# Performance work log

Hardware: AMD Instinct MI355X
Metric: run time of the kernel (lower is better)

The kernel has to match this reference:

```python
import math
import jax, jax.numpy as jnp
import numpy as np

NH, D, MULT, VOCAB, NLAYER = 4, 256, 128, 256, 2
N = MULT * D // NH  # 8192
EPS = 1e-5
THETA = 2.0 ** 16


def get_freqs(n):
    q = (jnp.arange(n, dtype=jnp.float32) // 2) * 2  # quantize(t, 2)
    return 1.0 / (THETA ** (q / n)) / (2 * math.pi)


def ln(x):
    # LayerNorm over last dim, no affine
    mu = jnp.mean(x, axis=-1, keepdims=True)
    var = jnp.mean((x - mu) ** 2, axis=-1, keepdims=True)
    return (x - mu) / jnp.sqrt(var + EPS)


def rope(phases, v):
    # phases: (T, N), v: (B, nh, T, N)
    ph = (phases % 1.0) * (2 * math.pi)
    c, s = jnp.cos(ph), jnp.sin(ph)
    v_rot = jnp.stack((-v[..., 1::2], v[..., ::2]), axis=-1).reshape(v.shape)
    return v * c + v_rot * s


def setup_inputs() -> dict:
    key = jax.random.key(0)
    ks = jax.random.split(key, 6)
    std = 0.02
    return {
        "idx": jax.random.randint(ks[0], (1, 2048), 0, VOCAB),
        "embed": jax.random.normal(ks[1], (VOCAB, D), jnp.float32) * std,
        "encoder": jax.random.normal(ks[2], (NH, D, N), jnp.float32) * std,
        "encoder_v": jax.random.normal(ks[3], (NH, D, N), jnp.float32) * std,
        "decoder": jax.random.normal(ks[4], (NH * N, D), jnp.float32) * std,
        "lm_head": jax.random.normal(ks[5], (D, VOCAB), jnp.float32) * std,
    }


def reference(idx, embed, encoder, encoder_v, decoder, lm_head):
    B, T = idx.shape
    freqs = get_freqs(N)  # (N,)
    phases = jnp.arange(T, dtype=jnp.float32)[:, None] * freqs[None, :]  # (T, N)
    # strictly-lower-triangular causal mask (tril diagonal=-1)
    t = jnp.arange(T)
    mask = (t[:, None] > t[None, :]).astype(jnp.float32)  # (T, T)

    x = ln(embed[idx][:, None])  # (B, 1, T, D)
    for _ in range(NLAYER):
        x_sparse = jax.nn.relu(jnp.einsum('bltd,hdn->bhtn', x, encoder))  # (B,nh,T,N)
        QR = rope(phases, x_sparse)
        scores = jnp.einsum('bhtn,bhsn->bhts', QR, QR) * mask  # (B,nh,T,T)
        yKV = ln(jnp.einsum('bhts,blsd->bhtd', scores, x))  # (B,nh,T,D)
        y_sparse = jax.nn.relu(jnp.einsum('bhtd,hdn->bhtn', yKV, encoder_v))
        xy = x_sparse * y_sparse  # (B,nh,T,N)
        xy = xy.transpose(0, 2, 1, 3).reshape(B, 1, T, NH * N)
        yMLP = xy @ decoder  # (B,1,T,D)
        x = ln(x + ln(yMLP))
    logits = x[:, 0] @ lm_head  # (B,T,vocab)
    return logits
```

## Files before the change

kernel.cpp:

```cpp
#include <hip/hip_runtime.h>
#include <hip/hip_bf16.h>
#include <math.h>

typedef unsigned short u16;
typedef unsigned int u32;
typedef __attribute__((ext_vector_type(8))) short short8;
typedef __attribute__((ext_vector_type(4))) float f32x4;

__device__ __forceinline__ u16 f2b(float f) {
  u32 u = __builtin_bit_cast(u32, f);
  u = (u + 0x7fffu + ((u >> 16) & 1u)) >> 16;
  return (u16)u;
}
__device__ __forceinline__ float b2f(u16 s) {
  return __builtin_bit_cast(float, (u32)s << 16);
}

__device__ __forceinline__ void ld_g2l(const u16* g, u16* l) {
  __builtin_amdgcn_global_load_lds(
      (const __attribute__((address_space(1))) unsigned int*)g,
      (__attribute__((address_space(3))) unsigned int*)l, 16, 0, 0);
}

__device__ __forceinline__ float rope_frev(int n) {
  return exp2f((float)(-(n & ~1)) * (1.0f / 512.0f)) * 0.15915494f;
}
__device__ __forceinline__ void rope_cs_fast(float frev, int t, float& c, float& s) {
  float ph = (float)t * frev;
  ph -= floorf(ph);
#if __has_builtin(__builtin_amdgcn_sinf) && __has_builtin(__builtin_amdgcn_cosf)
  s = __builtin_amdgcn_sinf(ph);
  c = __builtin_amdgcn_cosf(ph);
#else
  __sincosf(ph * 6.2831853f, &s, &c);
#endif
}

__device__ __forceinline__ void gemm_core(
    const u16* __restrict__ A, const u16* __restrict__ B,
    int lda, int ldb, int Klen, int kb, int bm, int bn,
    u16* __restrict__ As, u16* __restrict__ Bs, f32x4 (&acc)[4][4])
{
  int tid = threadIdx.x;
  int w = tid >> 6, lane = tid & 63;
  int srow = (w << 4) + (lane >> 2);
  int scol = (lane & 3) << 3;
  const u16* ga0 = A + (long)(bm * 128 + srow) * lda + kb + scol;
  const u16* ga1 = ga0 + (long)64 * lda;
  const u16* gb0 = B + (long)(bn * 128 + srow) * ldb + kb + scol;
  const u16* gb1 = gb0 + (long)64 * ldb;
  u16* la0 = As + (w << 9);  u16* la1 = la0 + 2048;
  u16* lb0 = Bs + (w << 9);  u16* lb1 = lb0 + 2048;

  int wm = (w >> 1) << 6, wn = (w & 1) << 6;
  int lane15 = lane & 15, quad = lane >> 4;
  const u16* ar = As + (wm + lane15) * 32 + quad * 8;
  const u16* br = Bs + (wn + lane15) * 32 + quad * 8;

#pragma unroll
  for (int i = 0; i < 4; i++)
#pragma unroll
    for (int j = 0; j < 4; j++) { f32x4 z = {0.f, 0.f, 0.f, 0.f}; acc[i][j] = z; }

  for (int k = 0; k < Klen; k += 64) {
    ld_g2l(ga0 + k, la0);
    ld_g2l(ga1 + k, la1);
    ld_g2l(gb0 + k, lb0);
    ld_g2l(gb1 + k, lb1);
    ld_g2l(ga0 + k + 32, la0 + 4096);
    ld_g2l(ga1 + k + 32, la1 + 4096);
    ld_g2l(gb0 + k + 32, lb0 + 4096);
    ld_g2l(gb1 + k + 32, lb1 + 4096);
    __syncthreads();
#pragma unroll
    for (int h = 0; h < 2; h++) {
      short8 af[4], bfr[4];
#pragma unroll
      for (int mt = 0; mt < 4; mt++) af[mt] = *(const short8*)(ar + h * 4096 + mt * 16 * 32);
#pragma unroll
      for (int nt = 0; nt < 4; nt++) bfr[nt] = *(const short8*)(br + h * 4096 + nt * 16 * 32);
#pragma unroll
      for (int mt = 0; mt < 4; mt++)
#pragma unroll
        for (int nt = 0; nt < 4; nt++)
          acc[mt][nt] = __builtin_amdgcn_mfma_f32_16x16x32_bf16(af[mt], bfr[nt], acc[mt][nt], 0, 0, 0);
    }
    __syncthreads();
  }
}

template<int EPI>
__global__ __launch_bounds__(256, 2) void gemm_bt(
    const u16* __restrict__ A, const u16* __restrict__ B, void* __restrict__ C,
    int K, int lda, int ldb, int ldc, int nsplits, long aB, long bB, long cB,
    int tri)
{
  __shared__ __align__(16) u16 As[2 * 128 * 32];
  __shared__ __align__(16) u16 Bs[2 * 128 * 32];
  int bn = blockIdx.x, bm = blockIdx.y;
  int batch = blockIdx.z / nsplits, sp = blockIdx.z % nsplits;
  int Klen = K / nsplits, kb = sp * Klen;
  if (tri) {
    int kend = (bm + 1) * 128;
    if (kb >= kend) return;
    if (kb + Klen > kend) Klen = kend - kb;
  }

  f32x4 acc[4][4];
  gemm_core(A + (long)batch * aB, B + (long)batch * bB, lda, ldb, Klen, kb, bm, bn, As, Bs, acc);

  int lane = threadIdx.x & 63, w = threadIdx.x >> 6;
  int wm = (w >> 1) << 6, wn = (w & 1) << 6;
  int lane15 = lane & 15, quad = lane >> 4;

  float frev[4] = {0.f, 0.f, 0.f, 0.f};
  if (EPI == 1 || EPI == 4) {
#pragma unroll
    for (int nt = 0; nt < 4; nt++)
      frev[nt] = rope_frev(bn * 128 + wn + nt * 16 + lane15);
  }

#pragma unroll
  for (int mt = 0; mt < 4; mt++)
#pragma unroll
    for (int nt = 0; nt < 4; nt++) {
      int gn = bn * 128 + wn + nt * 16 + lane15;
#pragma unroll
      for (int r = 0; r < 4; r++) {
        int gm = bm * 128 + wm + mt * 16 + quad * 4 + r;
        float v = acc[mt][nt][r];
        long ci = (long)batch * cB + (long)gm * ldc + gn;
        if (EPI == 0) {
          ((float*)C)[ci] = v;
        } else if (EPI == 1) {
          float rv = fmaxf(v, 0.f);
          float ro = __shfl_xor(rv, 1);
          float c, s; rope_cs_fast(frev[nt], gm, c, s);
          float out = (gn & 1) ? (rv * c + ro * s) : (rv * c - ro * s);
          ((u16*)C)[ci] = f2b(out);
        } else if (EPI == 3) {
          atomicAdd(&((float*)C)[ci], v);
        } else if (EPI == 4) {
          u16* Cp = (u16*)C;
          float q = b2f(Cp[ci]);
          float qo = __shfl_xor(q, 1);
          float c, s; rope_cs_fast(frev[nt], gm, c, s);
          float xs = (gn & 1) ? (q * c - qo * s) : (q * c + qo * s);
          Cp[ci] = f2b(fmaxf(v, 0.f) * xs);
        }
      }
    }
}

#define SC_BAR   __builtin_amdgcn_s_barrier()
#define SC_LGKM0 asm volatile("s_waitcnt lgkmcnt(0)" ::: "memory")
#define SC_LGKM8 asm volatile("s_waitcnt lgkmcnt(8)" ::: "memory")
#define SC_VMF   do { asm volatile("s_waitcnt vmcnt(4)" ::: "memory"); \
                      __builtin_amdgcn_sched_barrier(0); } while (0)
#define SC_P1    __builtin_amdgcn_s_setprio(1)
#define SC_P0    __builtin_amdgcn_s_setprio(0)

#define DSA(Ab, mh) { \
  _Pragma("unroll") for (int mt = 0; mt < 4; mt++) { \
    aA[mt][0] = *(const short8*)((Ab) + ((mh) * 64 + mt * 16) * 64 + koff0); \
    aA[mt][1] = *(const short8*)((Ab) + ((mh) * 64 + mt * 16) * 64 + koff1); } }

#define DSB(Bb, nh, dst) { \
  _Pragma("unroll") for (int nt = 0; nt < 2; nt++) { \
    dst[nt][0] = *(const short8*)((Bb) + ((nh) * 32 + nt * 16) * 64 + koff0); \
    dst[nt][1] = *(const short8*)((Bb) + ((nh) * 32 + nt * 16) * 64 + koff1); } }

#define MMA(MH, NH, BB) { \
  _Pragma("unroll") for (int mt = 0; mt < 4; mt++) \
  _Pragma("unroll") for (int nt = 0; nt < 2; nt++) { \
    acc[(MH)*4+mt][(NH)*2+nt] = __builtin_amdgcn_mfma_f32_16x16x32_bf16( \
        aA[mt][0], BB[nt][0], acc[(MH)*4+mt][(NH)*2+nt], 0, 0, 0); \
    acc[(MH)*4+mt][(NH)*2+nt] = __builtin_amdgcn_mfma_f32_16x16x32_bf16( \
        aA[mt][1], BB[nt][1], acc[(MH)*4+mt][(NH)*2+nt], 0, 0, 0); } }

__global__ __launch_bounds__(512, 1) void gemm_scores8(
    const u16* __restrict__ QR, u16* __restrict__ S, int T, int ntri)
{
  __shared__ __align__(16) u16 Abuf[2][256 * 64];
  __shared__ __align__(16) u16 Bbuf[2][256 * 64];

  int total = gridDim.x;
  int lin = blockIdx.x;
  int cpx = total >> 3, rr = total & 7;
  int xcd = lin & 7, ii = lin >> 3;
  int c = (xcd < rr) ? xcd * (cpx + 1) + ii
                     : rr * (cpx + 1) + (xcd - rr) * cpx + ii;
  int zh = c / ntri, q = c % ntri;

  int bm = (int)((sqrtf(8.f * (float)q + 1.f) - 1.f) * 0.5f);
  while ((bm + 1) * (bm + 2) / 2 <= q) bm++;
  while (bm * (bm + 1) / 2 > q) bm--;
  int bn = q - bm * (bm + 1) / 2;

  const u16* Q = QR + (long)zh * (long)T * 8192;
  u16* Sb = S + (long)zh * (long)T * T;

  int tid = threadIdx.x;
  int w = tid >> 6, lane = tid & 63;
  int wr = w >> 2, wc = w & 3;
  int lane15 = lane & 15, quad = lane >> 4;
  int swz = lane15 & 7;
  int koff0 = ((quad) ^ swz) << 3;
  int koff1 = ((4 + quad) ^ swz) << 3;

  const u16* gA = Q + (long)(bm * 256) * 8192;
  const u16* gB = Q + (long)(bn * 256) * 8192;

  const u16* A0 = &Abuf[0][(wr * 128 + lane15) * 64];
  const u16* A1 = &Abuf[1][(wr * 128 + lane15) * 64];
  const u16* B0 = &Bbuf[0][(wc * 64 + lane15) * 64];
  const u16* B1 = &Bbuf[1][(wc * 64 + lane15) * 64];

  int sr = lane >> 3, sc = lane & 7;
  long g_sk = (long)sr * 8192 + ((sc ^ sr) << 3);
  int l_base = (w * 16) * 64;
  long g_wrow = (long)(w * 16) * 8192;

  auto STG = [&](const u16* gHalfBase, u16* lHalfBase, int kt) {
    const u16* g = gHalfBase + g_wrow + g_sk + kt * 64;
    u16* l = lHalfBase + l_base;
    ld_g2l(g, l);
    ld_g2l(g + (long)8 * 8192, l + 8 * 64);
  };

  f32x4 acc[8][4];
#pragma unroll
  for (int i2 = 0; i2 < 8; i2++)
#pragma unroll
    for (int j = 0; j < 4; j++) { f32x4 z = {0.f, 0.f, 0.f, 0.f}; acc[i2][j] = z; }

  const long HSTEP = (long)128 * 8192;

  STG(gA, &Abuf[0][0], 0); STG(gA + HSTEP, &Abuf[0][128 * 64], 0);
  STG(gB, &Bbuf[0][0], 0); STG(gB + HSTEP, &Bbuf[0][128 * 64], 0);
  STG(gB, &Bbuf[1][0], 1); STG(gB + HSTEP, &Bbuf[1][128 * 64], 1);
  SC_VMF;
  SC_BAR;

  const int nkt = 8192 / 64;
  for (int i = 0; i < nkt / 2; i++) {
    int kt1 = 2 * i + 1;
    int kt2 = 2 * i + 2; if (kt2 > nkt - 1) kt2 = nkt - 1;
    int kt3 = 2 * i + 3; if (kt3 > nkt - 1) kt3 = nkt - 1;
    short8 aA[4][2], bb0[2][2], bb1[2][2];

    DSA(A0, 0); DSB(B0, 0, bb0);
    STG(gA, &Abuf[1][0], kt1);
    SC_LGKM8; SC_BAR; SC_LGKM0; SC_P1; MMA(0, 0, bb0); SC_P0; SC_BAR;
    DSB(B0, 1, bb1);
    STG(gA + HSTEP, &Abuf[1][128 * 64], kt1);
    SC_BAR; SC_LGKM0; SC_P1; MMA(0, 1, bb1); SC_P0; SC_BAR;
    DSA(A0, 1);
    STG(gB, &Bbuf[0][0], kt2);
    SC_BAR; SC_LGKM0; SC_P1; MMA(1, 1, bb1); SC_P0; SC_BAR;
    STG(gB + HSTEP, &Bbuf[0][128 * 64], kt2);
    SC_VMF; SC_BAR; SC_LGKM0; SC_P1; MMA(1, 0, bb0); SC_P0; SC_BAR;

    DSA(A1, 0); DSB(B1, 0, bb0);
    STG(gA, &Abuf[0][0], kt2);
    SC_LGKM8; SC_BAR; SC_LGKM0; SC_P1; MMA(0, 0, bb0); SC_P0; SC_BAR;
    DSB(B1, 1, bb1);
    STG(gA + HSTEP, &Abuf[0][128 * 64], kt2);
    SC_BAR; SC_LGKM0; SC_P1; MMA(0, 1, bb1); SC_P0; SC_BAR;
    DSA(A1, 1);
    STG(gB, &Bbuf[1][0], kt3);
    SC_BAR; SC_LGKM0; SC_P1; MMA(1, 1, bb1); SC_P0; SC_BAR;
    STG(gB + HSTEP, &Bbuf[1][128 * 64], kt3);
    SC_VMF; SC_BAR; SC_LGKM0; SC_P1; MMA(1, 0, bb0); SC_P0; SC_BAR;
  }

#pragma unroll
  for (int mt = 0; mt < 8; mt++)
#pragma unroll
    for (int nt = 0; nt < 4; nt++) {
      int gn = bn * 256 + wc * 64 + nt * 16 + lane15;
#pragma unroll
      for (int r = 0; r < 4; r++) {
        int gm = bm * 256 + wr * 128 + mt * 16 + quad * 4 + r;
        Sb[(long)gm * T + gn] = f2b(gm > gn ? acc[mt][nt][r] : 0.f);
      }
    }
}

__global__ __launch_bounds__(256) void trans_f32_bf16(
    const float* __restrict__ src, u16* __restrict__ dst, int R, int C)
{
  __shared__ float tile[32][33];
  long off = (long)blockIdx.z * R * C;
  const float* s = src + off;
  u16* d = dst + off;
  int lx = threadIdx.x & 31, ly = threadIdx.x >> 5;
  int c = blockIdx.x * 32 + lx;
#pragma unroll
  for (int p = 0; p < 32; p += 8)
    tile[ly + p][lx] = s[(long)(blockIdx.y * 32 + ly + p) * C + c];
  __syncthreads();
  int rr = blockIdx.y * 32 + lx;
#pragma unroll
  for (int p = 0; p < 32; p += 8)
    d[(long)(blockIdx.x * 32 + ly + p) * R + rr] = f2b(tile[lx][ly + p]);
}

__device__ __forceinline__ float block_sum(float v, float* red) {
#pragma unroll
  for (int o = 32; o > 0; o >>= 1) v += __shfl_down(v, o, 64);
  int lane = threadIdx.x & 63, wid = threadIdx.x >> 6;
  if (lane == 0) red[wid] = v;
  __syncthreads();
  float r = red[0] + red[1] + red[2] + red[3];
  __syncthreads();
  return r;
}

__global__ __launch_bounds__(256) void embed_ln(
    const int* __restrict__ idx, const float* __restrict__ embed,
    float* __restrict__ x, u16* __restrict__ xb, u16* __restrict__ xT, int T)
{
  __shared__ float red[4];
  int t = blockIdx.x, d = threadIdx.x;
  float v = embed[(long)idx[t] * 256 + d];
  float mu = block_sum(v, red) * (1.f / 256.f);
  float c = v - mu;
  float var = block_sum(c * c, red) * (1.f / 256.f);
  float o = c * rsqrtf(var + 1e-5f);
  x[(long)t * 256 + d] = o;
  xb[(long)t * 256 + d] = f2b(o);
  xT[(long)d * T + t] = f2b(o);
}

__global__ __launch_bounds__(256) void row_ln(
    const float* __restrict__ in, u16* __restrict__ out)
{
  __shared__ float red[4];
  long row = blockIdx.x;
  int d = threadIdx.x;
  float v = in[row * 256 + d];
  float mu = block_sum(v, red) * (1.f / 256.f);
  float c = v - mu;
  float var = block_sum(c * c, red) * (1.f / 256.f);
  out[row * 256 + d] = f2b(c * rsqrtf(var + 1e-5f));
}

__global__ __launch_bounds__(256) void resid_ln(
    const float* __restrict__ yMLP, float* __restrict__ x,
    u16* __restrict__ xb, u16* __restrict__ xT, int T)
{
  __shared__ float red[4];
  int t = blockIdx.x, d = threadIdx.x;
  float y = yMLP[(long)t * 256 + d];
  float mu1 = block_sum(y, red) * (1.f / 256.f);
  float c1 = y - mu1;
  float var1 = block_sum(c1 * c1, red) * (1.f / 256.f);
  float l1 = c1 * rsqrtf(var1 + 1e-5f);
  float v = x[(long)t * 256 + d] + l1;
  float mu2 = block_sum(v, red) * (1.f / 256.f);
  float c2 = v - mu2;
  float var2 = block_sum(c2 * c2, red) * (1.f / 256.f);
  float o = c2 * rsqrtf(var2 + 1e-5f);
  x[(long)t * 256 + d] = o;
  xb[(long)t * 256 + d] = f2b(o);
  xT[(long)d * T + t] = f2b(o);
}

extern "C" void kernel_launch(void* const* d_in, const int* in_sizes, int n_in,
                              void* d_out, int out_size, void* d_ws, size_t ws_size,
                              hipStream_t stream) {
  const int*   idx       = (const int*)d_in[0];
  const float* embed     = (const float*)d_in[1];
  const float* encoder   = (const float*)d_in[2];
  const float* encoder_v = (const float*)d_in[3];
  const float* decoder   = (const float*)d_in[4];
  const float* lm_head   = (const float*)d_in[5];
  const int T = in_sizes[0];
  const int D = 256, NH = 4, Nn = 8192, V = 256;

  char* ws = (char*)d_ws;
  size_t off = 0;
  auto alloc = [&](size_t bytes) -> void* {
    void* p = ws + off; off += (bytes + 255) & ~(size_t)255; return p;
  };
  float* x_f32   = (float*)alloc((size_t)T * D * 4);
  float* yMLP    = (float*)alloc((size_t)T * D * 4);
  float* yKV_f32 = (float*)alloc((size_t)NH * T * D * 4);
  u16* x_b    = (u16*)alloc((size_t)T * D * 2);
  u16* xT     = (u16*)alloc((size_t)T * D * 2);
  u16* yKV_b  = (u16*)alloc((size_t)NH * T * D * 2);
  u16* lmT    = (u16*)alloc((size_t)D * V * 2);
  u16* encT   = (u16*)alloc((size_t)NH * Nn * D * 2);
  u16* encvT  = (u16*)alloc((size_t)NH * Nn * D * 2);
  u16* decT   = (u16*)alloc((size_t)D * NH * Nn * 2);
  size_t per_head = ((size_t)T * T * 2 + 256) + ((size_t)T * Nn * 2 + 256);
  int HB = 4;
  while (HB > 1 && off + (size_t)HB * per_head > ws_size) HB >>= 1;
  u16* scores = (u16*)alloc((size_t)HB * T * T * 2);
  u16* QRxy   = (u16*)alloc((size_t)HB * T * Nn * 2);
  if (off > ws_size) return;

  trans_f32_bf16<<<dim3(Nn / 32, D / 32, NH), 256, 0, stream>>>(encoder, encT, D, Nn);
  trans_f32_bf16<<<dim3(Nn / 32, D / 32, NH), 256, 0, stream>>>(encoder_v, encvT, D, Nn);
  trans_f32_bf16<<<dim3(D / 32, (NH * Nn) / 32, 1), 256, 0, stream>>>(decoder, decT, NH * Nn, D);
  trans_f32_bf16<<<dim3(V / 32, D / 32, 1), 256, 0, stream>>>(lm_head, lmT, D, V);

  embed_ln<<<T, 256, 0, stream>>>(idx, embed, x_f32, x_b, xT, T);

  const int nbm = T / 256, ntri = nbm * (nbm + 1) / 2;

  for (int l = 0; l < 2; l++) {
    hipMemsetAsync(yMLP, 0, (size_t)T * D * 4, stream);
    for (int h0 = 0; h0 < NH; h0 += HB) {
      gemm_bt<1><<<dim3(Nn / 128, T / 128, HB), 256, 0, stream>>>(
          x_b, encT + (size_t)h0 * Nn * D, QRxy,
          D, D, D, Nn, 1, 0L, (long)Nn * D, (long)T * Nn, 0);
      gemm_scores8<<<dim3(ntri * HB, 1, 1), 512, 0, stream>>>(QRxy, scores, T, ntri);
      hipMemsetAsync(yKV_f32, 0, (size_t)HB * T * D * 4, stream);
      gemm_bt<3><<<dim3(D / 128, T / 128, HB * 8), 256, 0, stream>>>(
          scores, xT, yKV_f32,
          T, T, T, D, 8, (long)T * T, 0L, (long)T * D, 1);
      row_ln<<<HB * T, 256, 0, stream>>>(yKV_f32, yKV_b);
      gemm_bt<4><<<dim3(Nn / 128, T / 128, HB), 256, 0, stream>>>(
          yKV_b, encvT + (size_t)h0 * Nn * D, QRxy,
          D, D, D, Nn, 1, (long)T * D, (long)Nn * D, (long)T * Nn, 0);
      gemm_bt<3><<<dim3(D / 128, T / 128, HB * 4), 256, 0, stream>>>(
          QRxy, decT + (size_t)h0 * Nn, yMLP,
          Nn, Nn, NH * Nn, D, 4, (long)T * Nn, (long)Nn, 0L, 0);
    }
    resid_ln<<<T, 256, 0, stream>>>(yMLP, x_f32, x_b, xT, T);
  }

  gemm_bt<0><<<dim3(V / 128, T / 128, 1), 256, 0, stream>>>(
      x_b, lmT, d_out, D, D, D, V, 1, 0L, 0L, 0L, 0);
}
```

Before: 1.138 ms.

## Split causal score GEMM into 128x256 tiles plus half-size diagonal tiles

The scores kernel now tiles each head's lower triangle as 64 off-diagonal 128x256 tiles plus 8 diagonal 128x128 tiles, instead of 36 256x256 tiles. This doubles the number of blocks, which should fill more of the compute units and balance load better. It also skips some work above the diagonal. In exchange, each block has a smaller A tile and less register-level reuse, and the templated core adds a second code path with different wait counts.

Result: slower. 1.233 ms (+8.3%).

```diff
diff --git a/kernel.cpp b/kernel.cpp
--- a/kernel.cpp
+++ b/kernel.cpp
@@ -155,136 +155,148 @@
 #define SC_BAR   __builtin_amdgcn_s_barrier()
 #define SC_LGKM0 asm volatile("s_waitcnt lgkmcnt(0)" ::: "memory")
 #define SC_LGKM8 asm volatile("s_waitcnt lgkmcnt(8)" ::: "memory")
-#define SC_VMF   do { asm volatile("s_waitcnt vmcnt(4)" ::: "memory"); \
-                      __builtin_amdgcn_sched_barrier(0); } while (0)
 #define SC_P1    __builtin_amdgcn_s_setprio(1)
 #define SC_P0    __builtin_amdgcn_s_setprio(0)
 
-#define DSA(Ab, mh) { \
-  _Pragma("unroll") for (int mt = 0; mt < 4; mt++) { \
-    aA[mt][0] = *(const short8*)((Ab) + ((mh) * 64 + mt * 16) * 64 + koff0); \
-    aA[mt][1] = *(const short8*)((Ab) + ((mh) * 64 + mt * 16) * 64 + koff1); } }
-
-#define DSB(Bb, nh, dst) { \
-  _Pragma("unroll") for (int nt = 0; nt < 2; nt++) { \
-    dst[nt][0] = *(const short8*)((Bb) + ((nh) * 32 + nt * 16) * 64 + koff0); \
-    dst[nt][1] = *(const short8*)((Bb) + ((nh) * 32 + nt * 16) * 64 + koff1); } }
-
-#define MMA(MH, NH, BB) { \
-  _Pragma("unroll") for (int mt = 0; mt < 4; mt++) \
-  _Pragma("unroll") for (int nt = 0; nt < 2; nt++) { \
-    acc[(MH)*4+mt][(NH)*2+nt] = __builtin_amdgcn_mfma_f32_16x16x32_bf16( \
-        aA[mt][0], BB[nt][0], acc[(MH)*4+mt][(NH)*2+nt], 0, 0, 0); \
-    acc[(MH)*4+mt][(NH)*2+nt] = __builtin_amdgcn_mfma_f32_16x16x32_bf16( \
-        aA[mt][1], BB[nt][1], acc[(MH)*4+mt][(NH)*2+nt], 0, 0, 0); } }
-
-__global__ __launch_bounds__(512, 1) void gemm_scores8(
-    const u16* __restrict__ QR, u16* __restrict__ S, int T, int ntri)
-{
-  __shared__ __align__(16) u16 Abuf[2][256 * 64];
+template<int NW>
+__device__ __forceinline__ void score_core(
+    const u16* __restrict__ gA, const u16* __restrict__ gB,
+    u16* __restrict__ Sb, int T, int rowBase, int colBase,
+    u16* __restrict__ Ab, u16* __restrict__ Bb)
+{
+  constexpr int MT = (NW == 256) ? 4 : 2;
+  constexpr int RW = (NW == 256) ? 64 : 32;
+  constexpr int WCN = NW / 64;
+
+  int tid = threadIdx.x, w = tid >> 6, lane = tid & 63;
+  int wc = w % WCN, wr = w / WCN;
+  int lane15 = lane & 15, quad = lane >> 4;
+  int swz = lane15 & 7;
+  int koff0 = (quad ^ swz) << 3;
+  int koff1 = ((4 + quad) ^ swz) << 3;
+
+  u16* A0 = Ab;               u16* A1 = Ab + 128 * 64;
+  u16* B0 = Bb;               u16* B1 = Bb + 256 * 64;
+  const u16* a0r = A0 + (wr * RW + lane15) * 64;
+  const u16* a1r = A1 + (wr * RW + lane15) * 64;
+  const u16* b0r = B0 + (wc * 64 + lane15) * 64;
+  const u16* b1r = B1 + (wc * 64 + lane15) * 64;
+
+  int sr = lane >> 3, sc = lane & 7;
+  long g_sk = (long)sr * 8192 + ((sc ^ sr) << 3);
+  int l_base = (w * 16) * 64;
+  long g_wrow = (long)(w * 16) * 8192;
+
+  auto STG = [&](const u16* gBase, u16* lBase, int kt) {
+    const u16* g = gBase + g_wrow + g_sk + (long)kt * 64;
+    u16* l = lBase + l_base;
+    ld_g2l(g, l);
+    ld_g2l(g + (long)8 * 8192, l + 8 * 64);
+  };
+
+#define SC_VMF do { if (NW == 256) { \
+    asm volatile("s_waitcnt vmcnt(4)" ::: "memory"); } else { \
+    asm volatile("s_waitcnt vmcnt(2)" ::: "memory"); } \
+    __builtin_amdgcn_sched_barrier(0); } while (0)
+
+#define RD_A(ar_) { _Pragma("unroll") for (int mt = 0; mt < MT; mt++) { \
+    aA[mt][0] = *(const short8*)((ar_) + mt * 16 * 64 + koff0); \
+    aA[mt][1] = *(const short8*)((ar_) + mt * 16 * 64 + koff1); } }
+
+#define RD_B(br_, nh_, dst) { _Pragma("unroll") for (int nt = 0; nt < 2; nt++) { \
+    dst[nt][0] = *(const short8*)((br_) + ((nh_) * 32 + nt * 16) * 64 + koff0); \
+    dst[nt][1] = *(const short8*)((br_) + ((nh_) * 32 + nt * 16) * 64 + koff1); } }
+
+#define MMA9(NH_, KF_, BB_) { _Pragma("unroll") for (int mt = 0; mt < MT; mt++) \
+    _Pragma("unroll") for (int nt = 0; nt < 2; nt++) \
+      acc[mt][(NH_) * 2 + nt] = __builtin_amdgcn_mfma_f32_16x16x32_bf16( \
+          aA[mt][KF_], BB_[nt][KF_], acc[mt][(NH_) * 2 + nt], 0, 0, 0); }
+
+  f32x4 acc[MT][4];
+#pragma unroll
+  for (int i = 0; i < MT; i++)
+#pragma unroll
+    for (int j = 0; j < 4; j++) { f32x4 z = {0.f, 0.f, 0.f, 0.f}; acc[i][j] = z; }
+
+  const long HS = (long)128 * 8192;
+
+  STG(gA, A0, 0);
+  STG(gB, B0, 0); if (NW == 256) STG(gB + HS, B0 + 128 * 64, 0);
+  STG(gB, B1, 1); if (NW == 256) STG(gB + HS, B1 + 128 * 64, 1);
+  SC_VMF;
+  SC_BAR;
+
+  for (int i = 0; i < 64; i++) {
+    int kt1 = 2 * i + 1;
+    int kt2 = 2 * i + 2; if (kt2 > 127) kt2 = 127;
+    int kt3 = 2 * i + 3; if (kt3 > 127) kt3 = 127;
+    short8 aA[MT][2], bb0[2][2], bb1[2][2];
+
+    RD_A(a0r); RD_B(b0r, 0, bb0);
+    STG(gA, A1, kt1);
+    SC_LGKM8; SC_BAR; SC_LGKM0; SC_P1; MMA9(0, 0, bb0); SC_P0; SC_BAR;
+    RD_B(b0r, 1, bb1);
+    SC_BAR; SC_LGKM0; SC_P1; MMA9(1, 0, bb1); SC_P0; SC_BAR;
+    STG(gB, B0, kt2);
+    SC_BAR; SC_P1; MMA9(1, 1, bb1); SC_P0; SC_BAR;
+    if (NW == 256) STG(gB + HS, B0 + 128 * 64, kt2);
+    SC_VMF; SC_BAR; SC_P1; MMA9(0, 1, bb0); SC_P0; SC_BAR;
+
+    RD_A(a1r); RD_B(b1r, 0, bb0);
+    STG(gA, A0, kt2);
+    SC_LGKM8; SC_BAR; SC_LGKM0; SC_P1; MMA9(0, 0, bb0); SC_P0; SC_BAR;
+    RD_B(b1r, 1, bb1);
+    SC_BAR; SC_LGKM0; SC_P1; MMA9(1, 0, bb1); SC_P0; SC_BAR;
+    STG(gB, B1, kt3);
+    SC_BAR; SC_P1; MMA9(1, 1, bb1); SC_P0; SC_BAR;
+    if (NW == 256) STG(gB + HS, B1 + 128 * 64, kt3);
+    SC_VMF; SC_BAR; SC_P1; MMA9(0, 1, bb0); SC_P0; SC_BAR;
+  }
+
+#pragma unroll
+  for (int mt = 0; mt < MT; mt++)
+#pragma unroll
+    for (int nt4 = 0; nt4 < 4; nt4++) {
+      int gn = colBase + wc * 64 + nt4 * 16 + lane15;
+#pragma unroll
+      for (int r = 0; r < 4; r++) {
+        int gm = rowBase + wr * RW + mt * 16 + quad * 4 + r;
+        Sb[(long)gm * T + gn] = f2b(gm > gn ? acc[mt][nt4][r] : 0.f);
+      }
+    }
+#undef SC_VMF
+#undef RD_A
+#undef RD_B
+#undef MMA9
+}
+
+__global__ __launch_bounds__(512, 1) void gemm_scores9(
+    const u16* __restrict__ QR, u16* __restrict__ S, int T)
+{
+  __shared__ __align__(16) u16 Abuf[2][128 * 64];
   __shared__ __align__(16) u16 Bbuf[2][256 * 64];
 
-  int total = gridDim.x;
-  int lin = blockIdx.x;
+  int total = gridDim.x, lin = blockIdx.x;
   int cpx = total >> 3, rr = total & 7;
   int xcd = lin & 7, ii = lin >> 3;
   int c = (xcd < rr) ? xcd * (cpx + 1) + ii
                      : rr * (cpx + 1) + (xcd - rr) * cpx + ii;
-  int zh = c / ntri, q = c % ntri;
-
-  int bm = (int)((sqrtf(8.f * (float)q + 1.f) - 1.f) * 0.5f);
-  while ((bm + 1) * (bm + 2) / 2 <= q) bm++;
-  while (bm * (bm + 1) / 2 > q) bm--;
-  int bn = q - bm * (bm + 1) / 2;
-
-  const u16* Q = QR + (long)zh * (long)T * 8192;
-  u16* Sb = S + (long)zh * (long)T * T;
-
-  int tid = threadIdx.x;
-  int w = tid >> 6, lane = tid & 63;
-  int wr = w >> 2, wc = w & 3;
-  int lane15 = lane & 15, quad = lane >> 4;
-  int swz = lane15 & 7;
-  int koff0 = ((quad) ^ swz) << 3;
-  int koff1 = ((4 + quad) ^ swz) << 3;
-
-  const u16* gA = Q + (long)(bm * 256) * 8192;
-  const u16* gB = Q + (long)(bn * 256) * 8192;
-
-  const u16* A0 = &Abuf[0][(wr * 128 + lane15) * 64];
-  const u16* A1 = &Abuf[1][(wr * 128 + lane15) * 64];
-  const u16* B0 = &Bbuf[0][(wc * 64 + lane15) * 64];
-  const u16* B1 = &Bbuf[1][(wc * 64 + lane15) * 64];
-
-  int sr = lane >> 3, sc = lane & 7;
-  long g_sk = (long)sr * 8192 + ((sc ^ sr) << 3);
-  int l_base = (w * 16) * 64;
-  long g_wrow = (long)(w * 16) * 8192;
-
-  auto STG = [&](const u16* gHalfBase, u16* lHalfBase, int kt) {
-    const u16* g = gHalfBase + g_wrow + g_sk + kt * 64;
-    u16* l = lHalfBase + l_base;
-    ld_g2l(g, l);
-    ld_g2l(g + (long)8 * 8192, l + 8 * 64);
-  };
-
-  f32x4 acc[8][4];
-#pragma unroll
-  for (int i2 = 0; i2 < 8; i2++)
-#pragma unroll
-    for (int j = 0; j < 4; j++) { f32x4 z = {0.f, 0.f, 0.f, 0.f}; acc[i2][j] = z; }
-
-  const long HSTEP = (long)128 * 8192;
-
-  STG(gA, &Abuf[0][0], 0); STG(gA + HSTEP, &Abuf[0][128 * 64], 0);
-  STG(gB, &Bbuf[0][0], 0); STG(gB + HSTEP, &Bbuf[0][128 * 64], 0);
-  STG(gB, &Bbuf[1][0], 1); STG(gB + HSTEP, &Bbuf[1][128 * 64], 1);
-  SC_VMF;
-  SC_BAR;
-
-  const int nkt = 8192 / 64;
-  for (int i = 0; i < nkt / 2; i++) {
-    int kt1 = 2 * i + 1;
-    int kt2 = 2 * i + 2; if (kt2 > nkt - 1) kt2 = nkt - 1;
-    int kt3 = 2 * i + 3; if (kt3 > nkt - 1) kt3 = nkt - 1;
-    short8 aA[4][2], bb0[2][2], bb1[2][2];
-
-    DSA(A0, 0); DSB(B0, 0, bb0);
-    STG(gA, &Abuf[1][0], kt1);
-    SC_LGKM8; SC_BAR; SC_LGKM0; SC_P1; MMA(0, 0, bb0); SC_P0; SC_BAR;
-    DSB(B0, 1, bb1);
-    STG(gA + HSTEP, &Abuf[1][128 * 64], kt1);
-    SC_BAR; SC_LGKM0; SC_P1; MMA(0, 1, bb1); SC_P0; SC_BAR;
-    DSA(A0, 1);
-    STG(gB, &Bbuf[0][0], kt2);
-    SC_BAR; SC_LGKM0; SC_P1; MMA(1, 1, bb1); SC_P0; SC_BAR;
-    STG(gB + HSTEP, &Bbuf[0][128 * 64], kt2);
-    SC_VMF; SC_BAR; SC_LGKM0; SC_P1; MMA(1, 0, bb0); SC_P0; SC_BAR;
-
-    DSA(A1, 0); DSB(B1, 0, bb0);
-    STG(gA, &Abuf[0][0], kt2);
-    SC_LGKM8; SC_BAR; SC_LGKM0; SC_P1; MMA(0, 0, bb0); SC_P0; SC_BAR;
-    DSB(B1, 1, bb1);
-    STG(gA + HSTEP, &Abuf[0][128 * 64], kt2);
-    SC_BAR; SC_LGKM0; SC_P1; MMA(0, 1, bb1); SC_P0; SC_BAR;
-    DSA(A1, 1);
-    STG(gB, &Bbuf[1][0], kt3);
-    SC_BAR; SC_LGKM0; SC_P1; MMA(1, 1, bb1); SC_P0; SC_BAR;
-    STG(gB + HSTEP, &Bbuf[1][128 * 64], kt3);
-    SC_VMF; SC_BAR; SC_LGKM0; SC_P1; MMA(1, 0, bb0); SC_P0; SC_BAR;
-  }
-
-#pragma unroll
-  for (int mt = 0; mt < 8; mt++)
-#pragma unroll
-    for (int nt = 0; nt < 4; nt++) {
-      int gn = bn * 256 + wc * 64 + nt * 16 + lane15;
-#pragma unroll
-      for (int r = 0; r < 4; r++) {
-        int gm = bm * 256 + wr * 128 + mt * 16 + quad * 4 + r;
-        Sb[(long)gm * T + gn] = f2b(gm > gn ? acc[mt][nt][r] : 0.f);
-      }
-    }
+  int head = c / 72, r72 = c % 72;
+
+  const u16* Q = QR + (long)head * (long)T * 8192;
+  u16* Sb = S + (long)head * (long)T * T;
+
+  if (r72 < 8) {
+    int n = r72;
+    score_core<128>(Q + (long)n * 256 * 8192, Q + (long)n * 256 * 8192,
+                    Sb, T, n * 256, n * 256, &Abuf[0][0], &Bbuf[0][0]);
+  } else {
+    int L = r72 - 8, n = 0;
+    while (L >= 15 - 2 * n) { L -= 15 - 2 * n; n++; }
+    int mrow = 2 * n + 1 + L;
+    score_core<256>(Q + (long)mrow * 128 * 8192, Q + (long)n * 256 * 8192,
+                    Sb, T, mrow * 128, n * 256, &Abuf[0][0], &Bbuf[0][0]);
+  }
 }
 
 __global__ __launch_bounds__(256) void trans_f32_bf16(
@@ -408,15 +420,13 @@
 
   embed_ln<<<T, 256, 0, stream>>>(idx, embed, x_f32, x_b, xT, T);
 
-  const int nbm = T / 256, ntri = nbm * (nbm + 1) / 2;
-
   for (int l = 0; l < 2; l++) {
     hipMemsetAsync(yMLP, 0, (size_t)T * D * 4, stream);
     for (int h0 = 0; h0 < NH; h0 += HB) {
       gemm_bt<1><<<dim3(Nn / 128, T / 128, HB), 256, 0, stream>>>(
           x_b, encT + (size_t)h0 * Nn * D, QRxy,
           D, D, D, Nn, 1, 0L, (long)Nn * D, (long)T * Nn, 0);
-      gemm_scores8<<<dim3(ntri * HB, 1, 1), 512, 0, stream>>>(QRxy, scores, T, ntri);
+      gemm_scores9<<<dim3(HB * 72, 1, 1), 512, 0, stream>>>(QRxy, scores, T);
       hipMemsetAsync(yKV_f32, 0, (size_t)HB * T * D * 4, stream);
       gemm_bt<3><<<dim3(D / 128, T / 128, HB * 8), 256, 0, stream>>>(
           scores, xT, yKV_f32,
```

## Split scores GEMM along K into three slices with fp32 atomic accumulation

Applied to the files above, without the earlier changes.

Adds a split-K variant of the causal scores GEMM. Each 256x256 lower-triangle tile is computed by three blocks covering K slices of 44/44/40 k-tiles, which accumulate into a zeroed fp32 buffer with atomicAdd. A separate kernel then applies the strict causal mask and converts to bf16. With T=2048 and HB=4 there are only 36*4=144 tile blocks at one block per CU, so the split is meant to fill the CUs better. The cost is an extra fp32 T×T buffer, a memset, atomic traffic and a conversion pass, and the result now depends on atomic ordering.

New measurement: 1.140 ms. Within noise of the previous version (+0.2%).

```diff
diff --git a/kernel.cpp b/kernel.cpp
--- a/kernel.cpp
+++ b/kernel.cpp
@@ -6,6 +6,7 @@
 typedef unsigned int u32;
 typedef __attribute__((ext_vector_type(8))) short short8;
 typedef __attribute__((ext_vector_type(4))) float f32x4;
+typedef __attribute__((ext_vector_type(4))) unsigned short u16x4;
 
 __device__ __forceinline__ u16 f2b(float f) {
   u32 u = __builtin_bit_cast(u32, f);
@@ -178,63 +179,103 @@
     acc[(MH)*4+mt][(NH)*2+nt] = __builtin_amdgcn_mfma_f32_16x16x32_bf16( \
         aA[mt][1], BB[nt][1], acc[(MH)*4+mt][(NH)*2+nt], 0, 0, 0); } }
 
+#define SCORES_K_LOOP(kb, nkt) \
+  for (int i = 0; i < (nkt) / 2; i++) { \
+    int kt1 = (kb) + 2 * i + 1; \
+    int kt2 = 2 * i + 2; if (kt2 > (nkt) - 1) kt2 = (nkt) - 1; kt2 += (kb); \
+    int kt3 = 2 * i + 3; if (kt3 > (nkt) - 1) kt3 = (nkt) - 1; kt3 += (kb); \
+    short8 aA[4][2], bb0[2][2], bb1[2][2]; \
+     \
+    DSA(A0, 0); DSB(B0, 0, bb0); \
+    STG(gA, &Abuf[1][0], kt1); \
+    SC_LGKM8; SC_BAR; SC_LGKM0; SC_P1; MMA(0, 0, bb0); SC_P0; SC_BAR; \
+     \
+    DSB(B0, 1, bb1); \
+    STG(gA + HSTEP, &Abuf[1][128 * 64], kt1); \
+    SC_BAR; SC_LGKM0; SC_P1; MMA(0, 1, bb1); SC_P0; SC_BAR; \
+     \
+    DSA(A0, 1); \
+    STG(gB, &Bbuf[0][0], kt2); \
+    SC_BAR; SC_LGKM0; SC_P1; MMA(1, 1, bb1); SC_P0; SC_BAR; \
+     \
+    STG(gB + HSTEP, &Bbuf[0][128 * 64], kt2); \
+    SC_VMF; SC_BAR; SC_LGKM0; SC_P1; MMA(1, 0, bb0); SC_P0; SC_BAR; \
+     \
+    DSA(A1, 0); DSB(B1, 0, bb0); \
+    STG(gA, &Abuf[0][0], kt2); \
+    SC_LGKM8; SC_BAR; SC_LGKM0; SC_P1; MMA(0, 0, bb0); SC_P0; SC_BAR; \
+     \
+    DSB(B1, 1, bb1); \
+    STG(gA + HSTEP, &Abuf[0][128 * 64], kt2); \
+    SC_BAR; SC_LGKM0; SC_P1; MMA(0, 1, bb1); SC_P0; SC_BAR; \
+     \
+    DSA(A1, 1); \
+    STG(gB, &Bbuf[1][0], kt3); \
+    SC_BAR; SC_LGKM0; SC_P1; MMA(1, 1, bb1); SC_P0; SC_BAR; \
+     \
+    STG(gB + HSTEP, &Bbuf[1][128 * 64], kt3); \
+    SC_VMF; SC_BAR; SC_LGKM0; SC_P1; MMA(1, 0, bb0); SC_P0; SC_BAR; \
+  }
+
+#define SCORES_SETUP \
+  int tid = threadIdx.x; \
+  int w = tid >> 6, lane = tid & 63; \
+  int wr = w >> 2, wc = w & 3; \
+  int lane15 = lane & 15, quad = lane >> 4; \
+  int swz = lane15 & 7; \
+  int koff0 = ((quad) ^ swz) << 3; \
+  int koff1 = ((4 + quad) ^ swz) << 3; \
+  const u16* gA = Q + (long)(bm * 256) * 8192; \
+  const u16* gB = Q + (long)(bn * 256) * 8192; \
+  const u16* A0 = &Abuf[0][(wr * 128 + lane15) * 64]; \
+  const u16* A1 = &Abuf[1][(wr * 128 + lane15) * 64]; \
+  const u16* B0 = &Bbuf[0][(wc * 64 + lane15) * 64]; \
+  const u16* B1 = &Bbuf[1][(wc * 64 + lane15) * 64]; \
+  int sr = lane >> 3, sc = lane & 7; \
+  long g_sk = (long)sr * 8192 + ((sc ^ sr) << 3); \
+  int l_base = (w * 16) * 64; \
+  long g_wrow = (long)(w * 16) * 8192; \
+  auto STG = [&](const u16* gHalfBase, u16* lHalfBase, int kt) { \
+    const u16* g = gHalfBase + g_wrow + g_sk + (long)kt * 64; \
+    u16* l = lHalfBase + l_base; \
+    ld_g2l(g, l); \
+    ld_g2l(g + (long)8 * 8192, l + 8 * 64); \
+  }; \
+  f32x4 acc[8][4]; \
+  _Pragma("unroll") \
+  for (int i2 = 0; i2 < 8; i2++) \
+  _Pragma("unroll") \
+    for (int j = 0; j < 4; j++) { f32x4 z = {0.f, 0.f, 0.f, 0.f}; acc[i2][j] = z; } \
+  const long HSTEP = (long)128 * 8192;
+
+__device__ __forceinline__ void tri_decode(int q, int& bm, int& bn) {
+  bm = (int)((sqrtf(8.f * (float)q + 1.f) - 1.f) * 0.5f);
+  while ((bm + 1) * (bm + 2) / 2 <= q) bm++;
+  while (bm * (bm + 1) / 2 > q) bm--;
+  bn = q - bm * (bm + 1) / 2;
+}
+
+__device__ __forceinline__ int xcd_remap(int lin, int total) {
+  int cpx = total >> 3, rr = total & 7;
+  int xcd = lin & 7, ii = lin >> 3;
+  return (xcd < rr) ? xcd * (cpx + 1) + ii
+                    : rr * (cpx + 1) + (xcd - rr) * cpx + ii;
+}
+
 __global__ __launch_bounds__(512, 1) void gemm_scores8(
     const u16* __restrict__ QR, u16* __restrict__ S, int T, int ntri)
 {
   __shared__ __align__(16) u16 Abuf[2][256 * 64];
   __shared__ __align__(16) u16 Bbuf[2][256 * 64];
 
-  int total = gridDim.x;
-  int lin = blockIdx.x;
-  int cpx = total >> 3, rr = total & 7;
-  int xcd = lin & 7, ii = lin >> 3;
-  int c = (xcd < rr) ? xcd * (cpx + 1) + ii
-                     : rr * (cpx + 1) + (xcd - rr) * cpx + ii;
+  int c = xcd_remap(blockIdx.x, gridDim.x);
   int zh = c / ntri, q = c % ntri;
-
-  int bm = (int)((sqrtf(8.f * (float)q + 1.f) - 1.f) * 0.5f);
-  while ((bm + 1) * (bm + 2) / 2 <= q) bm++;
-  while (bm * (bm + 1) / 2 > q) bm--;
-  int bn = q - bm * (bm + 1) / 2;
+  int bm, bn; tri_decode(q, bm, bn);
 
   const u16* Q = QR + (long)zh * (long)T * 8192;
   u16* Sb = S + (long)zh * (long)T * T;
 
-  int tid = threadIdx.x;
-  int w = tid >> 6, lane = tid & 63;
-  int wr = w >> 2, wc = w & 3;
-  int lane15 = lane & 15, quad = lane >> 4;
-  int swz = lane15 & 7;
-  int koff0 = ((quad) ^ swz) << 3;
-  int koff1 = ((4 + quad) ^ swz) << 3;
-
-  const u16* gA = Q + (long)(bm * 256) * 8192;
-  const u16* gB = Q + (long)(bn * 256) * 8192;
-
-  const u16* A0 = &Abuf[0][(wr * 128 + lane15) * 64];
-  const u16* A1 = &Abuf[1][(wr * 128 + lane15) * 64];
-  const u16* B0 = &Bbuf[0][(wc * 64 + lane15) * 64];
-  const u16* B1 = &Bbuf[1][(wc * 64 + lane15) * 64];
-
-  int sr = lane >> 3, sc = lane & 7;
-  long g_sk = (long)sr * 8192 + ((sc ^ sr) << 3);
-  int l_base = (w * 16) * 64;
-  long g_wrow = (long)(w * 16) * 8192;
-
-  auto STG = [&](const u16* gHalfBase, u16* lHalfBase, int kt) {
-    const u16* g = gHalfBase + g_wrow + g_sk + kt * 64;
-    u16* l = lHalfBase + l_base;
-    ld_g2l(g, l);
-    ld_g2l(g + (long)8 * 8192, l + 8 * 64);
-  };
-
-  f32x4 acc[8][4];
-#pragma unroll
-  for (int i2 = 0; i2 < 8; i2++)
-#pragma unroll
-    for (int j = 0; j < 4; j++) { f32x4 z = {0.f, 0.f, 0.f, 0.f}; acc[i2][j] = z; }
-
-  const long HSTEP = (long)128 * 8192;
+  SCORES_SETUP
 
   STG(gA, &Abuf[0][0], 0); STG(gA + HSTEP, &Abuf[0][128 * 64], 0);
   STG(gB, &Bbuf[0][0], 0); STG(gB + HSTEP, &Bbuf[0][128 * 64], 0);
@@ -242,37 +283,7 @@
   SC_VMF;
   SC_BAR;
 
-  const int nkt = 8192 / 64;
-  for (int i = 0; i < nkt / 2; i++) {
-    int kt1 = 2 * i + 1;
-    int kt2 = 2 * i + 2; if (kt2 > nkt - 1) kt2 = nkt - 1;
-    int kt3 = 2 * i + 3; if (kt3 > nkt - 1) kt3 = nkt - 1;
-    short8 aA[4][2], bb0[2][2], bb1[2][2];
-
-    DSA(A0, 0); DSB(B0, 0, bb0);
-    STG(gA, &Abuf[1][0], kt1);
-    SC_LGKM8; SC_BAR; SC_LGKM0; SC_P1; MMA(0, 0, bb0); SC_P0; SC_BAR;
-    DSB(B0, 1, bb1);
-    STG(gA + HSTEP, &Abuf[1][128 * 64], kt1);
-    SC_BAR; SC_LGKM0; SC_P1; MMA(0, 1, bb1); SC_P0; SC_BAR;
-    DSA(A0, 1);
-    STG(gB, &Bbuf[0][0], kt2);
-    SC_BAR; SC_LGKM0; SC_P1; MMA(1, 1, bb1); SC_P0; SC_BAR;
-    STG(gB + HSTEP, &Bbuf[0][128 * 64], kt2);
-    SC_VMF; SC_BAR; SC_LGKM0; SC_P1; MMA(1, 0, bb0); SC_P0; SC_BAR;
-
-    DSA(A1, 0); DSB(B1, 0, bb0);
-    STG(gA, &Abuf[0][0], kt2);
-    SC_LGKM8; SC_BAR; SC_LGKM0; SC_P1; MMA(0, 0, bb0); SC_P0; SC_BAR;
-    DSB(B1, 1, bb1);
-    STG(gA + HSTEP, &Abuf[0][128 * 64], kt2);
-    SC_BAR; SC_LGKM0; SC_P1; MMA(0, 1, bb1); SC_P0; SC_BAR;
-    DSA(A1, 1);
-    STG(gB, &Bbuf[1][0], kt3);
-    SC_BAR; SC_LGKM0; SC_P1; MMA(1, 1, bb1); SC_P0; SC_BAR;
-    STG(gB + HSTEP, &Bbuf[1][128 * 64], kt3);
-    SC_VMF; SC_BAR; SC_LGKM0; SC_P1; MMA(1, 0, bb0); SC_P0; SC_BAR;
-  }
+  SCORES_K_LOOP(0, 128)
 
 #pragma unroll
   for (int mt = 0; mt < 8; mt++)
@@ -285,6 +296,71 @@
         Sb[(long)gm * T + gn] = f2b(gm > gn ? acc[mt][nt][r] : 0.f);
       }
     }
+}
+
+__global__ __launch_bounds__(512, 1) void gemm_scores_k3(
+    const u16* __restrict__ QR, float* __restrict__ Sf, int T, int ntri)
+{
+  __shared__ __align__(16) u16 Abuf[2][256 * 64];
+  __shared__ __align__(16) u16 Bbuf[2][256 * 64];
+
+  int c = xcd_remap(blockIdx.x, gridDim.x);
+  int sp = c % 3, c2 = c / 3;
+  int zh = c2 / ntri, q = c2 % ntri;
+  int bm, bn; tri_decode(q, bm, bn);
+
+  int kb = sp * 44;
+  int nkt = (sp == 2) ? 40 : 44;
+
+  const u16* Q = QR + (long)zh * (long)T * 8192;
+  float* Sb = Sf + (long)zh * (long)T * T;
+
+  SCORES_SETUP
+
+  STG(gA, &Abuf[0][0], kb); STG(gA + HSTEP, &Abuf[0][128 * 64], kb);
+  STG(gB, &Bbuf[0][0], kb); STG(gB + HSTEP, &Bbuf[0][128 * 64], kb);
+  STG(gB, &Bbuf[1][0], kb + 1); STG(gB + HSTEP, &Bbuf[1][128 * 64], kb + 1);
+  SC_VMF;
+  SC_BAR;
+
+  SCORES_K_LOOP(kb, nkt)
+
+#pragma unroll
+  for (int mt = 0; mt < 8; mt++)
+#pragma unroll
+    for (int nt = 0; nt < 4; nt++) {
+      int gn = bn * 256 + wc * 64 + nt * 16 + lane15;
+#pragma unroll
+      for (int r = 0; r < 4; r++) {
+        int gm = bm * 256 + wr * 128 + mt * 16 + quad * 4 + r;
+        atomicAdd(&Sb[(long)gm * T + gn], acc[mt][nt][r]);
+      }
+    }
+}
+
+__global__ __launch_bounds__(256) void tril_cvt(
+    const float* __restrict__ Sf, u16* __restrict__ Sb, int T, int ntri)
+{
+  int bx = blockIdx.x;
+  int tl = bx >> 3, chunk = bx & 7;
+  int zh = tl / ntri, q = tl % ntri;
+  int bm, bn; tri_decode(q, bm, bn);
+  const float* f = Sf + (long)zh * (long)T * T;
+  u16* b = Sb + (long)zh * (long)T * T;
+  int tid = threadIdx.x;
+  int rsub = tid >> 6;
+  int col = bn * 256 + (tid & 63) * 4;
+#pragma unroll
+  for (int it = 0; it < 8; it++) {
+    int row = bm * 256 + chunk * 32 + it * 4 + rsub;
+    long o = (long)row * T + col;
+    f32x4 v = *(const f32x4*)(f + o);
+    u16x4 w2;
+#pragma unroll
+    for (int r = 0; r < 4; r++)
+      w2[r] = (row > col + r) ? f2b(v[r]) : (u16)0;
+    *(u16x4*)(b + o) = w2;
+  }
 }
 
 __global__ __launch_bounds__(256) void trans_f32_bf16(
@@ -400,6 +476,11 @@
   u16* scores = (u16*)alloc((size_t)HB * T * T * 2);
   u16* QRxy   = (u16*)alloc((size_t)HB * T * Nn * 2);
   if (off > ws_size) return;
+  float* scoresF = nullptr;
+  {
+    size_t need = (size_t)HB * T * T * 4 + 256;
+    if (off + need <= ws_size) scoresF = (float*)alloc((size_t)HB * T * T * 4);
+  }
 
   trans_f32_bf16<<<dim3(Nn / 32, D / 32, NH), 256, 0, stream>>>(encoder, encT, D, Nn);
   trans_f32_bf16<<<dim3(Nn / 32, D / 32, NH), 256, 0, stream>>>(encoder_v, encvT, D, Nn);
@@ -416,7 +497,16 @@
       gemm_bt<1><<<dim3(Nn / 128, T / 128, HB), 256, 0, stream>>>(
           x_b, encT + (size_t)h0 * Nn * D, QRxy,
           D, D, D, Nn, 1, 0L, (long)Nn * D, (long)T * Nn, 0);
-      gemm_scores8<<<dim3(ntri * HB, 1, 1), 512, 0, stream>>>(QRxy, scores, T, ntri);
+      if (scoresF) {
+        hipMemsetAsync(scoresF, 0, (size_t)HB * T * T * 4, stream);
+        gemm_scores_k3<<<dim3(ntri * HB * 3, 1, 1), 512, 0, stream>>>(
+            QRxy, scoresF, T, ntri);
+        tril_cvt<<<dim3(HB * ntri * 8, 1, 1), 256, 0, stream>>>(
+            scoresF, scores, T, ntri);
+      } else {
+        gemm_scores8<<<dim3(ntri * HB, 1, 1), 512, 0, stream>>>(
+            QRxy, scores, T, ntri);
+      }
       hipMemsetAsync(yKV_f32, 0, (size_t)HB * T * D * 4, stream);
       gemm_bt<3><<<dim3(D / 128, T / 128, HB * 8), 256, 0, stream>>>(
           scores, xT, yKV_f32,
```
